# Kernel optimization log

Measured on AMD Instinct MI355X. Metric: run time of the kernel, lower is better.

Reference implementation:

```python
import jax, jax.numpy as jnp
import numpy as np

B, S, D = 4, 2048, 1024
NEG = -1.0e9


def setup_inputs() -> dict:
    key = jax.random.key(0)
    kq, kk, kv = jax.random.split(key, 3)
    query = jax.random.normal(kq, (B, S, D), dtype=jnp.float32)
    k = jax.random.normal(kk, (B, S, D), dtype=jnp.float32)
    value = jax.random.normal(kv, (B, S, D), dtype=jnp.float32)
    # causal mask: tril(ones(S,S)) with leading broadcast dim, as in the source script
    mask = jnp.tril(jnp.ones((S, S), dtype=jnp.int32))[None, :, :]
    return {"query": query, "key": k, "value": value, "mask": mask}


def reference(query, key, value, mask):
    d_q = query.shape[-1]
    scale = 1.0 / jnp.sqrt(jnp.float32(d_q))
    # [B, S, S] score matrix
    scores = jnp.einsum("bqd,bkd->bqk", query, key) * scale
    scores = jnp.where(mask == 0, jnp.float32(NEG), scores)
    attn = jax.nn.softmax(scores, axis=-1)
    out = jnp.einsum("bqk,bkd->bqd", attn, value)
    return (out, attn)
```

## Files before the change

kernel.cpp:

```cpp
#include <hip/hip_runtime.h>

#define Bn 4
#define Sn 2048
#define Dn 1024

typedef short bf16x8 __attribute__((ext_vector_type(8)));
typedef float f32x4 __attribute__((ext_vector_type(4)));

__device__ __forceinline__ unsigned f2bf(float x) {
    unsigned u = __float_as_uint(x);
    return (u + 0x7FFFu + ((u >> 16) & 1u)) >> 16;
}

__device__ __forceinline__ uint2 pack4(float4 v) {
    uint2 p;
    p.x = f2bf(v.x) | (f2bf(v.y) << 16);
    p.y = f2bf(v.z) | (f2bf(v.w) << 16);
    return p;
}

__device__ __forceinline__ void gl_lds16(const unsigned short* g, unsigned short* l) {
    __builtin_amdgcn_global_load_lds(
        (const __attribute__((address_space(1))) unsigned int*)g,
        (__attribute__((address_space(3))) unsigned int*)l, 16, 0, 0);
}

__global__ __launch_bounds__(256) void convert_qk_kernel(
    const float* __restrict__ Q, const float* __restrict__ K,
    unsigned short* __restrict__ Q16, unsigned short* __restrict__ K16) {
    size_t i = (size_t)blockIdx.x * 256 + threadIdx.x;
    float4 q = ((const float4*)Q)[i];
    ((uint2*)Q16)[i] = pack4(q);
    float4 k = ((const float4*)K)[i];
    ((uint2*)K16)[i] = pack4(k);
}

__global__ __launch_bounds__(256) void transpose_v_kernel(
    const float* __restrict__ V, unsigned short* __restrict__ Vt) {
    __shared__ unsigned short Ts[128 * 66];
    const int s0 = blockIdx.x * 128, d0 = blockIdx.y * 64, b = blockIdx.z;
    const float* Vb = V + ((size_t)b * Sn + s0) * Dn + d0;
    const int t = threadIdx.x;
#pragma unroll
    for (int i = 0; i < 8; i++) {
        int task = i * 256 + t;
        int r = task >> 4, c4 = task & 15;
        float4 v = *(const float4*)(Vb + (size_t)r * Dn + c4 * 4);
        *(uint2*)(&Ts[r * 66 + c4 * 4]) = pack4(v);
    }
    __syncthreads();
    unsigned short* Vtb = Vt + ((size_t)b * Dn + d0) * Sn + s0;
#pragma unroll
    for (int i = 0; i < 4; i++) {
        int task = i * 256 + t;
        int sc = task & 15, dr = task >> 4;
        unsigned short tmp[8];
#pragma unroll
        for (int j = 0; j < 8; j++) tmp[j] = Ts[(sc * 8 + j) * 66 + dr];
        uint4 u;
        u.x = tmp[0] | ((unsigned)tmp[1] << 16);
        u.y = tmp[2] | ((unsigned)tmp[3] << 16);
        u.z = tmp[4] | ((unsigned)tmp[5] << 16);
        u.w = tmp[6] | ((unsigned)tmp[7] << 16);
        *(uint4*)(&Vtb[(size_t)dr * Sn + sc * 8]) = u;
    }
}

__global__ __launch_bounds__(256) void qk_scores_kernel(
    const unsigned short* __restrict__ Q16, const unsigned short* __restrict__ K16,
    float* __restrict__ attn) {
    const int kt = blockIdx.x, qt = blockIdx.y, b = blockIdx.z;
    if (kt > qt) return;
    __shared__ unsigned short As[128 * 64];
    __shared__ unsigned short Bs[128 * 64];
    const unsigned short* Ag = Q16 + ((size_t)b * Sn + (size_t)qt * 128) * Dn;
    const unsigned short* Bg = K16 + ((size_t)b * Sn + (size_t)kt * 128) * Dn;
    const int t = threadIdx.x;
    const int w = t >> 6, lane = t & 63;
    const int wm = w >> 1, wn = w & 1;
    const int ml = lane & 15, quad = lane >> 4;
    const int lrow = lane >> 3, lcol = (lane & 7) * 8;
    f32x4 acc[4][4] = {};
    for (int d0 = 0; d0 < Dn; d0 += 64) {
#pragma unroll
        for (int j = 0; j < 4; j++) {
            int chunk = w * 4 + j;
            int row = chunk * 8 + lrow;
            gl_lds16(Ag + (size_t)row * Dn + d0 + lcol, As + chunk * 512);
            gl_lds16(Bg + (size_t)row * Dn + d0 + lcol, Bs + chunk * 512);
        }
        __syncthreads();
#pragma unroll
        for (int ko = 0; ko < 2; ko++) {
            bf16x8 af[4], bfr[4];
#pragma unroll
            for (int im = 0; im < 4; im++)
                af[im] = *(const bf16x8*)(&As[(wm * 64 + im * 16 + ml) * 64 + ko * 32 + quad * 8]);
#pragma unroll
            for (int in = 0; in < 4; in++)
                bfr[in] = *(const bf16x8*)(&Bs[(wn * 64 + in * 16 + ml) * 64 + ko * 32 + quad * 8]);
#pragma unroll
            for (int im = 0; im < 4; im++)
#pragma unroll
                for (int in = 0; in < 4; in++)
                    acc[im][in] = __builtin_amdgcn_mfma_f32_16x16x32_bf16(
                        af[im], bfr[in], acc[im][in], 0, 0, 0);
        }
        __syncthreads();
    }
    float* outp = attn + (size_t)b * Sn * Sn + ((size_t)qt * 128) * Sn + kt * 128;
#pragma unroll
    for (int im = 0; im < 4; im++)
#pragma unroll
        for (int in = 0; in < 4; in++)
#pragma unroll
            for (int r = 0; r < 4; r++) {
                int q = wm * 64 + im * 16 + quad * 4 + r;
                int k = wn * 64 + in * 16 + ml;
                outp[(size_t)q * Sn + k] = acc[im][in][r] * 0.03125f;
            }
}

__global__ __launch_bounds__(256) void softmax_kernel(
    float* __restrict__ attn, unsigned short* __restrict__ P16) {
    const int row = blockIdx.x;
    const int b = row >> 11, q = row & 2047;
    float* p = attn + (size_t)b * Sn * Sn + (size_t)q * Sn;
    unsigned short* p16 = P16 + (size_t)b * Sn * Sn + (size_t)q * Sn;
    __shared__ float buf[Sn];
    __shared__ float redA[4];
    __shared__ float redB[4];
    const int t = threadIdx.x;
    const int w = t >> 6, lane = t & 63;
    const int nv = q + 1;
    float lmax = -3.0e38f;
    for (int i = t; i < nv; i += 256) {
        float v = p[i];
        buf[i] = v;
        lmax = fmaxf(lmax, v);
    }
#pragma unroll
    for (int o = 32; o > 0; o >>= 1) lmax = fmaxf(lmax, __shfl_xor(lmax, o, 64));
    if (lane == 0) redA[w] = lmax;
    __syncthreads();
    const float m = fmaxf(fmaxf(redA[0], redA[1]), fmaxf(redA[2], redA[3]));
    float lsum = 0.f;
    for (int i = t; i < nv; i += 256) {
        float e = __expf(buf[i] - m);
        buf[i] = e;
        lsum += e;
    }
#pragma unroll
    for (int o = 32; o > 0; o >>= 1) lsum += __shfl_xor(lsum, o, 64);
    if (lane == 0) redB[w] = lsum;
    __syncthreads();
    const float inv = 1.0f / (redB[0] + redB[1] + redB[2] + redB[3]);
    for (int i = t; i < Sn; i += 256) {
        float v = (i < nv) ? buf[i] * inv : 0.0f;
        p[i] = v;
        p16[i] = (unsigned short)f2bf(v);
    }
}

__global__ __launch_bounds__(256) void pv_kernel(
    const unsigned short* __restrict__ P16, const unsigned short* __restrict__ Vt,
    float* __restrict__ out) {
    const int nt = blockIdx.x, qt = blockIdx.y, b = blockIdx.z;
    __shared__ unsigned short As[128 * 64];
    __shared__ unsigned short Bs[128 * 64];
    const unsigned short* Ag = P16 + ((size_t)b * Sn + (size_t)qt * 128) * Sn;
    const unsigned short* Bg = Vt + ((size_t)b * Dn + (size_t)nt * 128) * Sn;
    const int t = threadIdx.x;
    const int w = t >> 6, lane = t & 63;
    const int wm = w >> 1, wn = w & 1;
    const int ml = lane & 15, quad = lane >> 4;
    const int lrow = lane >> 3, lcol = (lane & 7) * 8;
    f32x4 acc[4][4] = {};
    const int nk = (qt + 1) * 128;
    for (int k0 = 0; k0 < nk; k0 += 64) {
#pragma unroll
        for (int j = 0; j < 4; j++) {
            int chunk = w * 4 + j;
            int row = chunk * 8 + lrow;
            gl_lds16(Ag + (size_t)row * Sn + k0 + lcol, As + chunk * 512);
            gl_lds16(Bg + (size_t)row * Sn + k0 + lcol, Bs + chunk * 512);
        }
        __syncthreads();
#pragma unroll
        for (int ko = 0; ko < 2; ko++) {
            bf16x8 af[4], bfr[4];
#pragma unroll
            for (int im = 0; im < 4; im++)
                af[im] = *(const bf16x8*)(&As[(wm * 64 + im * 16 + ml) * 64 + ko * 32 + quad * 8]);
#pragma unroll
            for (int in = 0; in < 4; in++)
                bfr[in] = *(const bf16x8*)(&Bs[(wn * 64 + in * 16 + ml) * 64 + ko * 32 + quad * 8]);
#pragma unroll
            for (int im = 0; im < 4; im++)
#pragma unroll
                for (int in = 0; in < 4; in++)
                    acc[im][in] = __builtin_amdgcn_mfma_f32_16x16x32_bf16(
                        af[im], bfr[in], acc[im][in], 0, 0, 0);
        }
        __syncthreads();
    }
    float* ob = out + (size_t)b * Sn * Dn + ((size_t)qt * 128) * Dn + nt * 128;
#pragma unroll
    for (int im = 0; im < 4; im++)
#pragma unroll
        for (int in = 0; in < 4; in++)
#pragma unroll
            for (int r = 0; r < 4; r++) {
                int q = wm * 64 + im * 16 + quad * 4 + r;
                int n = wn * 64 + in * 16 + ml;
                ob[(size_t)q * Dn + n] = acc[im][in][r];
            }
}

extern "C" void kernel_launch(void* const* d_in, const int* in_sizes, int n_in,
                              void* d_out, int out_size, void* d_ws, size_t ws_size,
                              hipStream_t stream) {
    const float* Q = (const float*)d_in[0];
    const float* K = (const float*)d_in[1];
    const float* V = (const float*)d_in[2];
    float* out = (float*)d_out;
    float* attn = out + (size_t)Bn * Sn * Dn;

    unsigned short* Q16 = (unsigned short*)d_ws;
    unsigned short* K16 = Q16 + (size_t)Bn * Sn * Dn;
    unsigned short* Vt  = K16 + (size_t)Bn * Sn * Dn;
    unsigned short* P16 = Vt  + (size_t)Bn * Dn * Sn;

    convert_qk_kernel<<<dim3((Bn * Sn * Dn) / (256 * 4)), 256, 0, stream>>>(Q, K, Q16, K16);
    transpose_v_kernel<<<dim3(Sn / 128, Dn / 64, Bn), 256, 0, stream>>>(V, Vt);

    qk_scores_kernel<<<dim3(16, 16, Bn), 256, 0, stream>>>(Q16, K16, attn);
    softmax_kernel<<<dim3(Bn * Sn), 256, 0, stream>>>(attn, P16);
    pv_kernel<<<dim3(8, 16, Bn), 256, 0, stream>>>(P16, Vt, out);
}
```

Measured before the change: 299.5 us.

## Store bf16 scores, double-buffer GEMM LDS, compact causal grid, reorder PV tiles

QK scores are now written as bf16 into a shared workspace instead of fp32 into the attn output, and softmax reads them back and overwrites them in place with bf16 probabilities. This cuts score write and read traffic. Both GEMM kernels now double-buffer their LDS tiles so the next global-to-LDS load overlaps the MFMA work, dropping one barrier per iteration. The QK grid is compacted to only the lower-triangular tiles via a triangular index decode, and the PV grid is linearized so the heaviest q-tiles launch first. The risk is lower score precision before softmax (bf16 rounding) and double the LDS footprint per block, which may reduce occupancy.

```diff
diff --git a/kernel.cpp b/kernel.cpp
--- a/kernel.cpp
+++ b/kernel.cpp
@@ -17,6 +17,10 @@
     p.x = f2bf(v.x) | (f2bf(v.y) << 16);
     p.y = f2bf(v.z) | (f2bf(v.w) << 16);
     return p;
+}
+
+__device__ __forceinline__ float bf2f(unsigned short s) {
+    return __uint_as_float((unsigned)s << 16);
 }
 
 __device__ __forceinline__ void gl_lds16(const unsigned short* g, unsigned short* l) {
@@ -68,11 +72,15 @@
 
 __global__ __launch_bounds__(256) void qk_scores_kernel(
     const unsigned short* __restrict__ Q16, const unsigned short* __restrict__ K16,
-    float* __restrict__ attn) {
-    const int kt = blockIdx.x, qt = blockIdx.y, b = blockIdx.z;
-    if (kt > qt) return;
-    __shared__ unsigned short As[128 * 64];
-    __shared__ unsigned short Bs[128 * 64];
+    unsigned short* __restrict__ S16) {
+    const int wid = blockIdx.x;
+    int qt = (int)((sqrtf(8.0f * wid + 1.0f) - 1.0f) * 0.5f);
+    while (qt * (qt + 1) / 2 > wid) qt--;
+    while ((qt + 1) * (qt + 2) / 2 <= wid) qt++;
+    const int kt = wid - qt * (qt + 1) / 2;
+    const int b = blockIdx.y;
+    __shared__ unsigned short As[2][128 * 64];
+    __shared__ unsigned short Bs[2][128 * 64];
     const unsigned short* Ag = Q16 + ((size_t)b * Sn + (size_t)qt * 128) * Dn;
     const unsigned short* Bg = K16 + ((size_t)b * Sn + (size_t)kt * 128) * Dn;
     const int t = threadIdx.x;
@@ -81,24 +89,31 @@
     const int ml = lane & 15, quad = lane >> 4;
     const int lrow = lane >> 3, lcol = (lane & 7) * 8;
     f32x4 acc[4][4] = {};
-    for (int d0 = 0; d0 < Dn; d0 += 64) {
+
+    auto stage = [&](int p, int d0) {
 #pragma unroll
         for (int j = 0; j < 4; j++) {
             int chunk = w * 4 + j;
             int row = chunk * 8 + lrow;
-            gl_lds16(Ag + (size_t)row * Dn + d0 + lcol, As + chunk * 512);
-            gl_lds16(Bg + (size_t)row * Dn + d0 + lcol, Bs + chunk * 512);
-        }
+            gl_lds16(Ag + (size_t)row * Dn + d0 + lcol, &As[p][chunk * 512]);
+            gl_lds16(Bg + (size_t)row * Dn + d0 + lcol, &Bs[p][chunk * 512]);
+        }
+    };
+
+    stage(0, 0);
+    int p = 0;
+    for (int d0 = 0; d0 < Dn; d0 += 64) {
         __syncthreads();
+        if (d0 + 64 < Dn) stage(p ^ 1, d0 + 64);
 #pragma unroll
         for (int ko = 0; ko < 2; ko++) {
             bf16x8 af[4], bfr[4];
 #pragma unroll
             for (int im = 0; im < 4; im++)
-                af[im] = *(const bf16x8*)(&As[(wm * 64 + im * 16 + ml) * 64 + ko * 32 + quad * 8]);
+                af[im] = *(const bf16x8*)(&As[p][(wm * 64 + im * 16 + ml) * 64 + ko * 32 + quad * 8]);
 #pragma unroll
             for (int in = 0; in < 4; in++)
-                bfr[in] = *(const bf16x8*)(&Bs[(wn * 64 + in * 16 + ml) * 64 + ko * 32 + quad * 8]);
+                bfr[in] = *(const bf16x8*)(&Bs[p][(wn * 64 + in * 16 + ml) * 64 + ko * 32 + quad * 8]);
 #pragma unroll
             for (int im = 0; im < 4; im++)
 #pragma unroll
@@ -106,9 +121,9 @@
                     acc[im][in] = __builtin_amdgcn_mfma_f32_16x16x32_bf16(
                         af[im], bfr[in], acc[im][in], 0, 0, 0);
         }
-        __syncthreads();
-    }
-    float* outp = attn + (size_t)b * Sn * Sn + ((size_t)qt * 128) * Sn + kt * 128;
+        p ^= 1;
+    }
+    unsigned short* outp = S16 + (size_t)b * Sn * Sn + ((size_t)qt * 128) * Sn + kt * 128;
 #pragma unroll
     for (int im = 0; im < 4; im++)
 #pragma unroll
@@ -117,16 +132,16 @@
             for (int r = 0; r < 4; r++) {
                 int q = wm * 64 + im * 16 + quad * 4 + r;
                 int k = wn * 64 + in * 16 + ml;
-                outp[(size_t)q * Sn + k] = acc[im][in][r] * 0.03125f;
+                outp[(size_t)q * Sn + k] = (unsigned short)f2bf(acc[im][in][r] * 0.03125f);
             }
 }
 
 __global__ __launch_bounds__(256) void softmax_kernel(
-    float* __restrict__ attn, unsigned short* __restrict__ P16) {
+    unsigned short* __restrict__ SP16, float* __restrict__ attn) {
     const int row = blockIdx.x;
     const int b = row >> 11, q = row & 2047;
-    float* p = attn + (size_t)b * Sn * Sn + (size_t)q * Sn;
-    unsigned short* p16 = P16 + (size_t)b * Sn * Sn + (size_t)q * Sn;
+    unsigned short* sp = SP16 + (size_t)b * Sn * Sn + (size_t)q * Sn;
+    float* ap = attn + (size_t)b * Sn * Sn + (size_t)q * Sn;
     __shared__ float buf[Sn];
     __shared__ float redA[4];
     __shared__ float redB[4];
@@ -135,7 +150,7 @@
     const int nv = q + 1;
     float lmax = -3.0e38f;
     for (int i = t; i < nv; i += 256) {
-        float v = p[i];
+        float v = bf2f(sp[i]);
         buf[i] = v;
         lmax = fmaxf(lmax, v);
     }
@@ -157,17 +172,20 @@
     const float inv = 1.0f / (redB[0] + redB[1] + redB[2] + redB[3]);
     for (int i = t; i < Sn; i += 256) {
         float v = (i < nv) ? buf[i] * inv : 0.0f;
-        p[i] = v;
-        p16[i] = (unsigned short)f2bf(v);
+        ap[i] = v;
+        sp[i] = (unsigned short)f2bf(v);
     }
 }
 
 __global__ __launch_bounds__(256) void pv_kernel(
     const unsigned short* __restrict__ P16, const unsigned short* __restrict__ Vt,
     float* __restrict__ out) {
-    const int nt = blockIdx.x, qt = blockIdx.y, b = blockIdx.z;
-    __shared__ unsigned short As[128 * 64];
-    __shared__ unsigned short Bs[128 * 64];
+    const int id = blockIdx.x;
+    const int qt = 15 - (id >> 5);
+    const int rest = id & 31;
+    const int nt = rest & 7, b = rest >> 3;
+    __shared__ unsigned short As[2][128 * 64];
+    __shared__ unsigned short Bs[2][128 * 64];
     const unsigned short* Ag = P16 + ((size_t)b * Sn + (size_t)qt * 128) * Sn;
     const unsigned short* Bg = Vt + ((size_t)b * Dn + (size_t)nt * 128) * Sn;
     const int t = threadIdx.x;
@@ -177,24 +195,31 @@
     const int lrow = lane >> 3, lcol = (lane & 7) * 8;
     f32x4 acc[4][4] = {};
     const int nk = (qt + 1) * 128;
-    for (int k0 = 0; k0 < nk; k0 += 64) {
+
+    auto stage = [&](int p, int k0) {
 #pragma unroll
         for (int j = 0; j < 4; j++) {
             int chunk = w * 4 + j;
             int row = chunk * 8 + lrow;
-            gl_lds16(Ag + (size_t)row * Sn + k0 + lcol, As + chunk * 512);
-            gl_lds16(Bg + (size_t)row * Sn + k0 + lcol, Bs + chunk * 512);
-        }
+            gl_lds16(Ag + (size_t)row * Sn + k0 + lcol, &As[p][chunk * 512]);
+            gl_lds16(Bg + (size_t)row * Sn + k0 + lcol, &Bs[p][chunk * 512]);
+        }
+    };
+
+    stage(0, 0);
+    int p = 0;
+    for (int k0 = 0; k0 < nk; k0 += 64) {
         __syncthreads();
+        if (k0 + 64 < nk) stage(p ^ 1, k0 + 64);
 #pragma unroll
         for (int ko = 0; ko < 2; ko++) {
             bf16x8 af[4], bfr[4];
 #pragma unroll
             for (int im = 0; im < 4; im++)
-                af[im] = *(const bf16x8*)(&As[(wm * 64 + im * 16 + ml) * 64 + ko * 32 + quad * 8]);
+                af[im] = *(const bf16x8*)(&As[p][(wm * 64 + im * 16 + ml) * 64 + ko * 32 + quad * 8]);
 #pragma unroll
             for (int in = 0; in < 4; in++)
-                bfr[in] = *(const bf16x8*)(&Bs[(wn * 64 + in * 16 + ml) * 64 + ko * 32 + quad * 8]);
+                bfr[in] = *(const bf16x8*)(&Bs[p][(wn * 64 + in * 16 + ml) * 64 + ko * 32 + quad * 8]);
 #pragma unroll
             for (int im = 0; im < 4; im++)
 #pragma unroll
@@ -202,7 +227,7 @@
                     acc[im][in] = __builtin_amdgcn_mfma_f32_16x16x32_bf16(
                         af[im], bfr[in], acc[im][in], 0, 0, 0);
         }
-        __syncthreads();
+        p ^= 1;
     }
     float* ob = out + (size_t)b * Sn * Dn + ((size_t)qt * 128) * Dn + nt * 128;
 #pragma unroll
@@ -229,12 +254,12 @@
     unsigned short* Q16 = (unsigned short*)d_ws;
     unsigned short* K16 = Q16 + (size_t)Bn * Sn * Dn;
     unsigned short* Vt  = K16 + (size_t)Bn * Sn * Dn;
-    unsigned short* P16 = Vt  + (size_t)Bn * Dn * Sn;
+    unsigned short* SP16 = Vt + (size_t)Bn * Dn * Sn;
 
     convert_qk_kernel<<<dim3((Bn * Sn * Dn) / (256 * 4)), 256, 0, stream>>>(Q, K, Q16, K16);
     transpose_v_kernel<<<dim3(Sn / 128, Dn / 64, Bn), 256, 0, stream>>>(V, Vt);
 
-    qk_scores_kernel<<<dim3(16, 16, Bn), 256, 0, stream>>>(Q16, K16, attn);
-    softmax_kernel<<<dim3(Bn * Sn), 256, 0, stream>>>(attn, P16);
-    pv_kernel<<<dim3(8, 16, Bn), 256, 0, stream>>>(P16, Vt, out);
-}
+    qk_scores_kernel<<<dim3(136, Bn), 256, 0, stream>>>(Q16, K16, SP16);
+    softmax_kernel<<<dim3(Bn * Sn), 256, 0, stream>>>(SP16, attn);
+    pv_kernel<<<dim3(512), 256, 0, stream>>>(SP16, Vt, out);
+}
```

Result: faster. 290.8 us (-2.9%).
